# Optimization experiments

Hardware: AMD Instinct MI355X
Metric: run time of the kernel (lower is better)

Reference implementation:

```python
import jax, jax.numpy as jnp
import numpy as np
from jax import lax

HW = 96  # heatmap / image size, hardcoded in the module


def _conv(x, w, b, stride):
    # torch Conv2d: weight [O,I,kH,kW], padding=1
    y = lax.conv_general_dilated(x, w, (stride, stride), [(1, 1), (1, 1)],
                                 dimension_numbers=('NCHW', 'OIHW', 'NCHW'))
    return y + b[None, :, None, None]


def _deconv(x, w, b):
    # torch ConvTranspose2d(k=4, stride=2, padding=1): weight [I,O,kH,kW]
    # equivalent to conv with lhs_dilation=2, padding=k-1-p=2, flipped kernel, I/O swapped
    wf = jnp.flip(w, (-2, -1)).transpose(1, 0, 2, 3)  # [O,I,4,4]
    y = lax.conv_general_dilated(x, wf, (1, 1), [(2, 2), (2, 2)],
                                 lhs_dilation=(2, 2),
                                 dimension_numbers=('NCHW', 'OIHW', 'NCHW'))
    return y + b[None, :, None, None]


def _heatmap(landmarks_flat):
    # landmarks_flat: [B,T,136] -> vectorized scatter of 68 points per frame
    B, T, _ = landmarks_flat.shape
    BT = B * T
    lm = landmarks_flat.reshape(BT, 68, 2) * (HW - 1)
    idx = lm.astype(jnp.int32)          # torch .long() truncation (coords >= 0)
    x, y = idx[..., 0], idx[..., 1]
    valid = (y >= 0) & (y < HW) & (x >= 0) & (x < HW)
    y_s = jnp.where(valid, y, -1)       # out-of-range -> dropped by scatter
    x_s = jnp.where(valid, x, -1)
    bidx = jnp.broadcast_to(jnp.arange(BT)[:, None], (BT, 68))
    h = jnp.zeros((BT, HW, HW), dtype=landmarks_flat.dtype)
    h = h.at[bidx, y_s, x_s].set(1.0, mode='drop')
    return h[:, None, :, :]             # [BT,1,96,96]


def _forward(identity_image, landmark_sequence, w1, b1, w2, b2, w3, b3, w4, b4):
    B, T, _ = landmark_sequence.shape
    ident = jnp.broadcast_to(identity_image[:, None], (B, T, 3, HW, HW)).reshape(B * T, 3, HW, HW)
    hm = _heatmap(landmark_sequence)
    x = jnp.concatenate([ident, hm], axis=1)          # [BT,4,96,96]
    x = jax.nn.relu(_conv(x, w1, b1, 2))              # [BT,64,48,48]
    x = jax.nn.relu(_conv(x, w2, b2, 2))              # [BT,128,24,24]
    x = jax.nn.relu(_deconv(x, w3, b3))               # [BT,64,48,48]
    x = jnp.tanh(_deconv(x, w4, b4))                  # [BT,3,96,96]
    return x.reshape(B, T, 3, HW, HW)


def setup_inputs() -> dict:
    key = jax.random.key(0)
    ks = jax.random.split(key, 10)
    B, T = 8, 32
    identity_image = jax.random.normal(ks[0], (B, 3, HW, HW), dtype=jnp.float32)
    landmark_sequence = jax.random.uniform(ks[1], (B, T, 136), dtype=jnp.float32)
    s = 0.05
    return {
        'identity_image': identity_image,
        'landmark_sequence': landmark_sequence,
        'w1': jax.random.normal(ks[2], (64, 4, 4, 4), jnp.float32) * s,
        'b1': jnp.zeros((64,), jnp.float32),
        'w2': jax.random.normal(ks[3], (128, 64, 4, 4), jnp.float32) * s,
        'b2': jnp.zeros((128,), jnp.float32),
        'w3': jax.random.normal(ks[4], (128, 64, 4, 4), jnp.float32) * s,  # torch ConvTranspose layout [I,O,kH,kW]
        'b3': jnp.zeros((64,), jnp.float32),
        'w4': jax.random.normal(ks[5], (64, 3, 4, 4), jnp.float32) * s,
        'b4': jnp.zeros((3,), jnp.float32),
    }


def reference(identity_image, landmark_sequence, w1, b1, w2, b2, w3, b3, w4, b4):
    return _forward(identity_image, landmark_sequence, w1, b1, w2, b2, w3, b3, w4, b4)
```

## Files before the change

kernel.cpp:

```cpp
#include <hip/hip_runtime.h>

#define IDENTP_OFF 0u
#define HMP_OFF    470400u
#define ACT1CL_OFF 5488000u
#define ACT3P_OFF  470400u
#define ACT2P_OFF  90684800u
#define W2B_OFF    134987136u
#define W3B_OFF    135249280u
#define W1B_OFF    135642496u
#define W4C_OFF    135650688u

using short8  = __attribute__((ext_vector_type(8))) short;
using floatx4 = __attribute__((ext_vector_type(4))) float;
union UV { uint4 u; short8 s; };

static __device__ __forceinline__ float bf2f(unsigned short u) {
  union { unsigned int i; float f; } v; v.i = ((unsigned int)u) << 16; return v.f;
}
static __device__ __forceinline__ unsigned short f2bf(float f) {
  union { float f; unsigned int i; } v; v.f = f;
  unsigned int x = v.i;
  return (unsigned short)((x + 0x7FFFu + ((x >> 16) & 1u)) >> 16);
}
static __device__ __forceinline__ uint4 pack8(const unsigned short* v) {
  uint4 p;
  p.x = (unsigned)v[0] | ((unsigned)v[1] << 16);
  p.y = (unsigned)v[2] | ((unsigned)v[3] << 16);
  p.z = (unsigned)v[4] | ((unsigned)v[5] << 16);
  p.w = (unsigned)v[6] | ((unsigned)v[7] << 16);
  return p;
}
static __device__ __forceinline__ float ftanh(float x) {
  x = fminf(fmaxf(x, -10.f), 10.f);
  float e = __expf(2.f * x);
  return (e - 1.f) * __builtin_amdgcn_rcpf(e + 1.f);
}

__global__ __launch_bounds__(256) void prep_kernel(
    const float* __restrict__ lm, const float* __restrict__ ident,
    const float* __restrict__ w1, const float* __restrict__ w2,
    const float* __restrict__ w3, const float* __restrict__ w4,
    unsigned short* __restrict__ identp, unsigned short* __restrict__ hmp,
    unsigned short* __restrict__ w1b, unsigned short* __restrict__ w2t,
    unsigned short* __restrict__ w3t, unsigned short* __restrict__ w4c,
    unsigned short* __restrict__ act1cl, unsigned short* __restrict__ act2p) {
  int bid = blockIdx.x, tid = threadIdx.x;
  if (bid < 256) {
    unsigned int* h32 = (unsigned int*)(hmp + bid * 9800);
    for (int i = tid; i < 4900; i += 256) h32[i] = 0u;
    __syncthreads();
    if (tid < 68) {
      float x = lm[bid * 136 + tid * 2 + 0] * 95.0f;
      float y = lm[bid * 136 + tid * 2 + 1] * 95.0f;
      int ix = (int)x, iy = (int)y;
      if (ix >= 0 && ix < 96 && iy >= 0 && iy < 96)
        hmp[bid * 9800 + (iy + 1) * 100 + (ix + 1)] = 0x3F80;
    }
  } else if (bid < 320) {
    int idx = (bid - 256) * 2048 + tid * 8;
    int kk = idx >> 12, rem = idx & 4095;
    int n = rem >> 5, e = rem & 31;
    unsigned short v[8];
#pragma unroll
    for (int j = 0; j < 8; j++) {
      int t = kk * 32 + e + j;
      int tap = t >> 6, ic = t & 63;
      v[j] = f2bf(w2[n * 1024 + ic * 16 + tap]);
    }
    *(uint4*)(w2t + idx) = pack8(v);
  } else if (bid < 416) {
    int idx = (bid - 320) * 2048 + tid * 8;
    int r = idx / 98304;
    int rem2 = idx - r * 98304;
    int kk = rem2 >> 12, rem3 = rem2 & 4095;
    int n = rem3 >> 5, e = rem3 & 31;
    int s = n >> 6, oc = n & 63;
    unsigned short v[8];
#pragma unroll
    for (int j = 0; j < 8; j++) {
      int k = kk * 32 + e + j;
      int tap = k >> 7, ic = k & 127;
      int dh = tap / 3, dw = tap - dh * 3;
      int a = 1 - dh, bb = s + 1 - dw;
      unsigned short val = 0;
      if (bb >= 0 && bb <= 1) {
        int kh = 2 * a + 1 - r, kw = 2 * bb + 1 - s;
        val = f2bf(w3[ic * 1024 + oc * 16 + kh * 4 + kw]);
      }
      v[j] = val;
    }
    *(uint4*)(w3t + idx) = pack8(v);
  } else if (bid < 440) {
    int bci = bid - 416;
    const float* src = ident + bci * 9216;
    unsigned short* dst = identp + bci * 9800;
    for (int i = tid; i < 9800; i += 256) {
      int row = i / 100, col = i - row * 100;
      bool in = (row >= 1) && (row <= 96) && (col >= 1) && (col <= 96);
      dst[i] = in ? f2bf(src[(row - 1) * 96 + (col - 1)]) : (unsigned short)0;
    }
  } else if (bid < 696) {
    unsigned short* base = act1cl + (size_t)(bid - 440) * 166400u;
    for (int c = tid; c < 1568; c += 256) {
      int cell = c >> 3, v = c & 7;
      int row, col;
      if (cell < 50) { row = 0; col = cell; }
      else if (cell < 100) { row = 49; col = cell - 50; }
      else if (cell < 148) { row = cell - 99; col = 0; }
      else { row = cell - 147; col = 49; }
      *(uint4*)(base + (row * 52 + col) * 64 + v * 8) = (uint4){0, 0, 0, 0};
    }
  } else if (bid < 952) {
    uint4* b4p = (uint4*)(act2p + (size_t)(bid - 696) * 86528u);
    uint4 z = {0, 0, 0, 0};
    for (int c = tid; c < 1600; c += 256) {
      int cell = c >> 4, v = c & 15;
      int row, col;
      if (cell < 26) { row = 0; col = cell; }
      else if (cell < 52) { row = 25; col = cell - 26; }
      else if (cell < 76) { row = cell - 51; col = 0; }
      else { row = cell - 75; col = 25; }
      b4p[(row * 26 + col) * 16 + v] = z;
    }
  } else if (bid == 952) {
    int e = tid * 16;
    unsigned short v[16];
#pragma unroll
    for (int q = 0; q < 4; q++) {
      float4 f = *(const float4*)(w1 + e + q * 4);
      v[q * 4 + 0] = f2bf(f.x); v[q * 4 + 1] = f2bf(f.y);
      v[q * 4 + 2] = f2bf(f.z); v[q * 4 + 3] = f2bf(f.w);
    }
    *(uint4*)(w1b + e) = pack8(v);
    *(uint4*)(w1b + e + 8) = pack8(v + 8);
  } else {
    for (int idx = tid; idx < 9216; idx += 256) {
      int n = idx / 576, k = idx - n * 576;
      int t = k >> 6, ic = k & 63;
      int dh = t / 3, dw = t - dh * 3;
      unsigned short val = 0;
      if (n < 12) {
        int cls = n / 3, oc = n - cls * 3;
        int r = cls >> 1, s = cls & 1;
        int a = r - dh + 1, b = s - dw + 1;
        if (a >= 0 && a < 2 && b >= 0 && b < 2) {
          int kh = 2 * a + 1 - r, kw = 2 * b + 1 - s;
          val = f2bf(w4[ic * 48 + oc * 16 + kh * 4 + kw]);
        }
      }
      w4c[idx] = val;
    }
  }
}

__global__ __launch_bounds__(256) void conv1_kernel(
    const unsigned short* __restrict__ identp, const unsigned short* __restrict__ hmp,
    const unsigned short* __restrict__ w1b, const float* __restrict__ b1,
    unsigned short* __restrict__ act1cl) {
  __shared__ unsigned short stage[4608];
  int tid = threadIdx.x;
  int bx = blockIdx.x, bt = blockIdx.y;
  int b = bt >> 5;
  int wave = tid >> 6, lane = tid & 63, quad = lane >> 4, l16 = lane & 15;
  int px0 = bx * 64 + wave * 16;
  int pxa = px0 + l16;
  int oh = pxa / 48, ow = pxa % 48;

  floatx4 acc[4];
#pragma unroll
  for (int nt = 0; nt < 4; nt++) acc[nt] = (floatx4){0.f, 0.f, 0.f, 0.f};

#pragma unroll
  for (int kk = 0; kk < 2; kk++) {
    int k0 = kk * 32 + quad * 8;
    int ic = k0 >> 4, khp = (k0 >> 3) & 1;
    const unsigned short* src = (ic < 3) ? identp + (b * 3 + ic) * 9800
                                         : hmp + bt * 9800;
    const unsigned short* p = src + (2 * oh + khp * 2) * 100 + 2 * ow;
    UV a;
    a.u.x = *(const unsigned int*)(p);
    a.u.y = *(const unsigned int*)(p + 2);
    a.u.z = *(const unsigned int*)(p + 100);
    a.u.w = *(const unsigned int*)(p + 102);
#pragma unroll
    for (int nt = 0; nt < 4; nt++) {
      UV bv;
      bv.u = *(const uint4*)(w1b + (nt * 16 + l16) * 64 + kk * 32 + quad * 8);
      acc[nt] = __builtin_amdgcn_mfma_f32_16x16x32_bf16(a.s, bv.s, acc[nt], 0, 0, 0);
    }
  }

  float bias[4];
#pragma unroll
  for (int nt = 0; nt < 4; nt++) bias[nt] = b1[nt * 16 + l16];
  unsigned short* sw = stage + wave * 1152;
#pragma unroll
  for (int nt = 0; nt < 4; nt++)
#pragma unroll
    for (int reg = 0; reg < 4; reg++) {
      float v = fmaxf(acc[nt][reg] + bias[nt], 0.f);
      sw[(quad * 4 + reg) * 72 + nt * 16 + l16] = f2bf(v);
    }
  __syncthreads();
  int oh0 = px0 / 48, ow0 = px0 % 48;
  unsigned short* gout = act1cl + (size_t)bt * 166400u + ((oh0 + 1) * 52 + ow0 + 1) * 64;
#pragma unroll
  for (int it = 0; it < 8; it++) {
    int pl = it * 2 + (lane >> 5);
    unsigned int v = *(const unsigned int*)(sw + pl * 72 + (lane & 31) * 2);
    *(unsigned int*)(gout + pl * 64 + (lane & 31) * 2) = v;
  }
}

__global__ __launch_bounds__(256, 2) void conv2_kernel(
    const unsigned short* __restrict__ act1cl, const unsigned short* __restrict__ w2t,
    const float* __restrict__ b2, unsigned short* __restrict__ act2p) {
  __shared__ unsigned short Blds[2][128 * 40];
  int tid = threadIdx.x;
  int bx = blockIdx.x, bt = blockIdx.y;
  int wave = tid >> 6, lane = tid & 63, quad = lane >> 4, l16 = lane & 15;
  const unsigned short* frame = act1cl + (size_t)bt * 166400u;
  const unsigned short* abase[3];
#pragma unroll
  for (int mf = 0; mf < 3; mf++) {
    int px = bx * 192 + wave * 48 + mf * 16 + l16;
    int oh = px / 24, ow = px % 24;
    abase[mf] = frame + ((2 * oh) * 52 + 2 * ow) * 64 + quad * 8;
  }
  const unsigned short* bptr = w2t + tid * 16;
  unsigned short* sdst = &Blds[0][0] + (tid >> 1) * 40 + (tid & 1) * 16;

  floatx4 acc[3][8];
#pragma unroll
  for (int mf = 0; mf < 3; mf++)
#pragma unroll
    for (int nt = 0; nt < 8; nt++) acc[mf][nt] = (floatx4){0.f, 0.f, 0.f, 0.f};

  {
    uint4 s0 = *(const uint4*)(bptr);
    uint4 s1 = *(const uint4*)(bptr + 8);
    *(uint4*)(sdst) = s0;
    *(uint4*)(sdst + 8) = s1;
  }
  UV a_cur[3], a_nxt[3];
#pragma unroll
  for (int mf = 0; mf < 3; mf++) a_cur[mf].u = *(const uint4*)(abase[mf]);
  __syncthreads();

#pragma unroll 2
  for (int kk = 0; kk < 32; kk++) {
    int cur = kk & 1;
    UV bf[8];
#pragma unroll
    for (int nt = 0; nt < 8; nt++)
      bf[nt].u = *(const uint4*)(&Blds[cur][(nt * 16 + l16) * 40 + quad * 8]);
    uint4 ns0, ns1;
    if (kk < 31) {
      const unsigned short* p = bptr + (kk + 1) * 4096;
      ns0 = *(const uint4*)(p);
      ns1 = *(const uint4*)(p + 8);
      int tap = (kk + 1) >> 1, ic0 = ((kk + 1) & 1) * 32;
      int kh = tap >> 2, kw = tap & 3;
      int aoff = (kh * 52 + kw) * 64 + ic0;
#pragma unroll
      for (int mf = 0; mf < 3; mf++) a_nxt[mf].u = *(const uint4*)(abase[mf] + aoff);
    }
#pragma unroll
    for (int mf = 0; mf < 3; mf++)
#pragma unroll
      for (int nt = 0; nt < 8; nt++)
        acc[mf][nt] = __builtin_amdgcn_mfma_f32_16x16x32_bf16(a_cur[mf].s, bf[nt].s, acc[mf][nt], 0, 0, 0);
    if (kk < 31) {
      unsigned short* d = sdst + (1 - cur) * 5120;
      *(uint4*)(d) = ns0;
      *(uint4*)(d + 8) = ns1;
    }
    __syncthreads();
#pragma unroll
    for (int mf = 0; mf < 3; mf++) a_cur[mf] = a_nxt[mf];
  }

  float bias[8];
#pragma unroll
  for (int nt = 0; nt < 8; nt++) bias[nt] = b2[nt * 16 + l16];
  unsigned short* sw = &Blds[0][0] + wave * 2176;
  unsigned short* obase = act2p + (size_t)bt * 86528u;
#pragma unroll
  for (int mf = 0; mf < 3; mf++) {
#pragma unroll
    for (int nt = 0; nt < 8; nt++)
#pragma unroll
      for (int reg = 0; reg < 4; reg++) {
        float v = fmaxf(acc[mf][nt][reg] + bias[nt], 0.f);
        sw[(quad * 4 + reg) * 136 + nt * 16 + l16] = f2bf(v);
      }
    __syncthreads();
#pragma unroll
    for (int it = 0; it < 16; it++) {
      unsigned int v = *(const unsigned int*)(sw + it * 136 + lane * 2);
      int px = bx * 192 + wave * 48 + mf * 16 + it;
      int oh = px / 24, ow = px % 24;
      *(unsigned int*)(obase + ((oh + 1) * 26 + ow + 1) * 128 + lane * 2) = v;
    }
    __syncthreads();
  }
}

__global__ __launch_bounds__(256, 2) void deconv3_kernel(
    const unsigned short* __restrict__ act2p, const unsigned short* __restrict__ w3t,
    const float* __restrict__ b3, unsigned short* __restrict__ act3p) {
  __shared__ unsigned short Blds[2][128 * 40];
  int tid = threadIdx.x;
  int bx = blockIdx.x, r = blockIdx.y, bt = blockIdx.z;
  int wave = tid >> 6, lane = tid & 63, quad = lane >> 4, l16 = lane & 15;
  const unsigned short* a2 = act2p + (size_t)bt * 86528u;
  unsigned short* a3 = act3p + (size_t)bt * 160000u;

  if (bx == 0 && r == 0) {
    uint4* hz = (uint4*)a3;
    uint4 z = {0, 0, 0, 0};
    for (int c = tid; c < 1568; c += 256) {
      int cell = c >> 3, v = c & 7;
      int row, col;
      if (cell < 50) { row = 0; col = cell; }
      else if (cell < 100) { row = 49; col = cell - 50; }
      else if (cell < 148) { row = cell - 99; col = 0; }
      else { row = cell - 147; col = 49; }
      hz[(row * 50 + col) * 8 + v] = z;
    }
  }

  const unsigned short* abase[3];
#pragma unroll
  for (int mf = 0; mf < 3; mf++) {
    int px = bx * 192 + wave * 48 + mf * 16 + l16;
    int i = px / 24, j = px % 24;
    abase[mf] = a2 + ((i + r) * 26 + j) * 128 + quad * 8;
  }
  const unsigned short* bptr = w3t + r * 98304 + tid * 16;
  unsigned short* sdst = &Blds[0][0] + (tid >> 1) * 40 + (tid & 1) * 16;

  floatx4 acc[3][8];
#pragma unroll
  for (int mf = 0; mf < 3; mf++)
#pragma unroll
    for (int nt = 0; nt < 8; nt++) acc[mf][nt] = (floatx4){0.f, 0.f, 0.f, 0.f};

  {
    uint4 s0 = *(const uint4*)(bptr);
    uint4 s1 = *(const uint4*)(bptr + 8);
    *(uint4*)(sdst) = s0;
    *(uint4*)(sdst + 8) = s1;
  }
  UV a_cur[3], a_nxt[3];
#pragma unroll
  for (int mf = 0; mf < 3; mf++) a_cur[mf].u = *(const uint4*)(abase[mf]);
  __syncthreads();

#pragma unroll 2
  for (int kk = 0; kk < 24; kk++) {
    int cur = kk & 1;
    UV bf[8];
#pragma unroll
    for (int nt = 0; nt < 8; nt++)
      bf[nt].u = *(const uint4*)(&Blds[cur][(nt * 16 + l16) * 40 + quad * 8]);
    uint4 ns0, ns1;
    if (kk < 23) {
      const unsigned short* p = bptr + (kk + 1) * 4096;
      ns0 = *(const uint4*)(p);
      ns1 = *(const uint4*)(p + 8);
      int tap = (kk + 1) >> 2, ic0 = ((kk + 1) & 3) * 32;
      int dh = tap / 3, dw = tap - dh * 3;
      int aoff = (dh * 26 + dw) * 128 + ic0;
#pragma unroll
      for (int mf = 0; mf < 3; mf++) a_nxt[mf].u = *(const uint4*)(abase[mf] + aoff);
    }
#pragma unroll
    for (int mf = 0; mf < 3; mf++)
#pragma unroll
      for (int nt = 0; nt < 8; nt++)
        acc[mf][nt] = __builtin_amdgcn_mfma_f32_16x16x32_bf16(a_cur[mf].s, bf[nt].s, acc[mf][nt], 0, 0, 0);
    if (kk < 23) {
      unsigned short* d = sdst + (1 - cur) * 5120;
      *(uint4*)(d) = ns0;
      *(uint4*)(d + 8) = ns1;
    }
    __syncthreads();
#pragma unroll
    for (int mf = 0; mf < 3; mf++) a_cur[mf] = a_nxt[mf];
  }

  float bias[8];
#pragma unroll
  for (int nt = 0; nt < 8; nt++) bias[nt] = b3[(nt * 16 + l16) & 63];
  unsigned short* sw = &Blds[0][0] + wave * 2176;
#pragma unroll
  for (int mf = 0; mf < 3; mf++) {
#pragma unroll
    for (int nt = 0; nt < 8; nt++)
#pragma unroll
      for (int reg = 0; reg < 4; reg++) {
        float v = fmaxf(acc[mf][nt][reg] + bias[nt], 0.f);
        sw[(quad * 4 + reg) * 136 + nt * 16 + l16] = f2bf(v);
      }
    __syncthreads();
#pragma unroll
    for (int it = 0; it < 16; it++) {
      unsigned int v = *(const unsigned int*)(sw + it * 136 + lane * 2);
      int px = bx * 192 + wave * 48 + mf * 16 + it;
      int i = px / 24, j = px % 24;
      *(unsigned int*)(a3 + ((2 * i + r + 1) * 50 + 2 * j + 1) * 64 + lane * 2) = v;
    }
    __syncthreads();
  }
}

__global__ __launch_bounds__(256) void deconv4_kernel(
    const unsigned short* __restrict__ act3p, const unsigned short* __restrict__ w4c,
    const float* __restrict__ b4, float* __restrict__ out) {
  __shared__ uint4 lds4[2400 + 1168];
  int tid = threadIdx.x;
  int wave = tid >> 6, lane = tid & 63, quad = lane >> 4, l16 = lane & 15;
  int bx = blockIdx.x, bt = blockIdx.y;
  int i0 = bx * 4;

  const uint4* src = (const uint4*)(act3p + (size_t)bt * 160000u + i0 * 3200);
#pragma unroll
  for (int v = 0; v < 10; v++) {
    int g = v * 256 + tid;
    if (g < 2400) {
      uint4 d = src[g];
      int row = g / 400;
      int rem = g - row * 400;
      int rec = rem >> 3, lc = rem & 7;
      lds4[row * 400 + rec * 8 + ((lc + rec) & 7)] = d;
    }
  }
  const uint4* wsrc = (const uint4*)w4c;
#pragma unroll
  for (int v = 0; v < 5; v++) {
    int g = v * 256 + tid;
    if (g < 1152) {
      uint4 d = wsrc[g];
      int n = g / 72, off = g - n * 72;
      lds4[2400 + n * 73 + off] = d;
    }
  }
  __syncthreads();

  const char* alds = (const char*)lds4;
  const char* blds = (const char*)(lds4 + 2400);

  UV bfr[18];
#pragma unroll
  for (int kk = 0; kk < 18; kk++)
    bfr[kk].u = *(const uint4*)(blds + l16 * 1168 + kk * 64 + quad * 16);

  int i = i0 + wave;
  int n = l16;
  int cls = n / 3, oc = n - cls * 3;
  int r = cls >> 1, s = cls & 1;
  float bias = (n < 12) ? b4[oc] : 0.f;
  int oh = 2 * i + r;

#pragma unroll
  for (int t3 = 0; t3 < 3; t3++) {
    int j0 = t3 * 16;
    floatx4 acc = (floatx4){0.f, 0.f, 0.f, 0.f};
#pragma unroll
    for (int kk = 0; kk < 18; kk++) {
      int par = kk & 1, tap = kk >> 1;
      int dh = tap / 3, dw = tap - dh * 3;
      int rec = j0 + dw + l16;
      int pc = (par * 4 + quad + rec) & 7;
      UV a;
      a.u = *(const uint4*)(alds + (wave + dh) * 6400 + rec * 128 + pc * 16);
      acc = __builtin_amdgcn_mfma_f32_16x16x32_bf16(a.s, bfr[kk].s, acc, 0, 0, 0);
    }
    if (n < 12) {
      float* obase = out + (size_t)bt * 27648u + oc * 9216 + oh * 96 + s;
#pragma unroll
      for (int reg = 0; reg < 4; reg++) {
        int jj = j0 + quad * 4 + reg;
        obase[2 * jj] = ftanh(acc[reg] + bias);
      }
    }
  }
}

extern "C" void kernel_launch(void* const* d_in, const int* in_sizes, int n_in,
                              void* d_out, int out_size, void* d_ws, size_t ws_size,
                              hipStream_t stream) {
  const float* ident = (const float*)d_in[0];
  const float* lm = (const float*)d_in[1];
  const float* w1 = (const float*)d_in[2];
  const float* b1 = (const float*)d_in[3];
  const float* w2 = (const float*)d_in[4];
  const float* b2 = (const float*)d_in[5];
  const float* w3 = (const float*)d_in[6];
  const float* b3 = (const float*)d_in[7];
  const float* w4 = (const float*)d_in[8];
  const float* b4 = (const float*)d_in[9];
  float* out = (float*)d_out;
  char* ws = (char*)d_ws;
  unsigned short* identp = (unsigned short*)(ws + IDENTP_OFF);
  unsigned short* hmp = (unsigned short*)(ws + HMP_OFF);
  unsigned short* act1cl = (unsigned short*)(ws + ACT1CL_OFF);
  unsigned short* act2p = (unsigned short*)(ws + ACT2P_OFF);
  unsigned short* act3p = (unsigned short*)(ws + ACT3P_OFF);
  unsigned short* w2t = (unsigned short*)(ws + W2B_OFF);
  unsigned short* w3t = (unsigned short*)(ws + W3B_OFF);
  unsigned short* w1b = (unsigned short*)(ws + W1B_OFF);
  unsigned short* w4c = (unsigned short*)(ws + W4C_OFF);

  prep_kernel<<<dim3(954), 256, 0, stream>>>(lm, ident, w1, w2, w3, w4, identp, hmp,
                                             w1b, w2t, w3t, w4c, act1cl, act2p);
  conv1_kernel<<<dim3(36, 256), 256, 0, stream>>>(identp, hmp, w1b, b1, act1cl);
  conv2_kernel<<<dim3(3, 256), 256, 0, stream>>>(act1cl, w2t, b2, act2p);
  deconv3_kernel<<<dim3(3, 2, 256), 256, 0, stream>>>(act2p, w3t, b3, act3p);
  deconv4_kernel<<<dim3(12, 256), 256, 0, stream>>>(act3p, w4c, b4, out);
}
```

Before: 319.3 us.

## Split deconv3 into four parity-class GEMMs with 2x2 taps, skipping zero-weight taps

The deconv3 kernel previously handled each output-row parity with a 3x3 tap window over both column parities, so its K dimension was padded with zeros. It now launches one block per (row parity, column parity) class using only the 4 real taps, which cuts K from 768 to 512 and N from 128 to 64 per block. The weight prep is rewritten to produce these per-class 2x2 weight matrices. Each class's weights are staged into LDS in two halves instead of a per-step double buffer, the launch grid becomes 12x256, and the 2-blocks-per-CU launch bound is dropped. In exchange there are more blocks, each doing less MFMA work per A-fragment load.

```diff
diff --git a/kernel.cpp b/kernel.cpp
--- a/kernel.cpp
+++ b/kernel.cpp
@@ -42,7 +42,7 @@
     const float* __restrict__ w3, const float* __restrict__ w4,
     unsigned short* __restrict__ identp, unsigned short* __restrict__ hmp,
     unsigned short* __restrict__ w1b, unsigned short* __restrict__ w2t,
-    unsigned short* __restrict__ w3t, unsigned short* __restrict__ w4c,
+    unsigned short* __restrict__ w3c, unsigned short* __restrict__ w4c,
     unsigned short* __restrict__ act1cl, unsigned short* __restrict__ act2p) {
   int bid = blockIdx.x, tid = threadIdx.x;
   if (bid < 256) {
@@ -68,28 +68,26 @@
       v[j] = f2bf(w2[n * 1024 + ic * 16 + tap]);
     }
     *(uint4*)(w2t + idx) = pack8(v);
+  } else if (bid < 384) {
+    int idx = (bid - 320) * 2048 + tid * 8;
+    int c = idx >> 15;
+    int rem = idx & 32767;
+    int kk = rem >> 11;
+    int rem2 = rem & 2047;
+    int n = rem2 >> 5;
+    int ep = rem2 & 31;
+    int r = c >> 1, s = c & 1;
+    unsigned short v[8];
+#pragma unroll
+    for (int j = 0; j < 8; j++) {
+      int k = kk * 32 + ep + j;
+      int tap = k >> 7, ic = k & 127;
+      int dh = tap >> 1, dw = tap & 1;
+      int kh = 3 - r - 2 * dh, kw = 3 - s - 2 * dw;
+      v[j] = f2bf(w3[ic * 1024 + n * 16 + kh * 4 + kw]);
+    }
+    *(uint4*)(w3c + idx) = pack8(v);
   } else if (bid < 416) {
-    int idx = (bid - 320) * 2048 + tid * 8;
-    int r = idx / 98304;
-    int rem2 = idx - r * 98304;
-    int kk = rem2 >> 12, rem3 = rem2 & 4095;
-    int n = rem3 >> 5, e = rem3 & 31;
-    int s = n >> 6, oc = n & 63;
-    unsigned short v[8];
-#pragma unroll
-    for (int j = 0; j < 8; j++) {
-      int k = kk * 32 + e + j;
-      int tap = k >> 7, ic = k & 127;
-      int dh = tap / 3, dw = tap - dh * 3;
-      int a = 1 - dh, bb = s + 1 - dw;
-      unsigned short val = 0;
-      if (bb >= 0 && bb <= 1) {
-        int kh = 2 * a + 1 - r, kw = 2 * bb + 1 - s;
-        val = f2bf(w3[ic * 1024 + oc * 16 + kh * 4 + kw]);
-      }
-      v[j] = val;
-    }
-    *(uint4*)(w3t + idx) = pack8(v);
   } else if (bid < 440) {
     int bci = bid - 416;
     const float* src = ident + bci * 9216;
@@ -306,21 +304,24 @@
   }
 }
 
-__global__ __launch_bounds__(256, 2) void deconv3_kernel(
-    const unsigned short* __restrict__ act2p, const unsigned short* __restrict__ w3t,
+__global__ __launch_bounds__(256) void deconv3_kernel(
+    const unsigned short* __restrict__ act2p, const unsigned short* __restrict__ w3c,
     const float* __restrict__ b3, unsigned short* __restrict__ act3p) {
-  __shared__ unsigned short Blds[2][128 * 40];
+  __shared__ uint4 lds[2560];
   int tid = threadIdx.x;
-  int bx = blockIdx.x, r = blockIdx.y, bt = blockIdx.z;
   int wave = tid >> 6, lane = tid & 63, quad = lane >> 4, l16 = lane & 15;
+
+  int bxc = blockIdx.x, bt = blockIdx.y;
+  int c = bxc & 3, bx = bxc >> 2;
+  int r = c >> 1, s = c & 1;
   const unsigned short* a2 = act2p + (size_t)bt * 86528u;
   unsigned short* a3 = act3p + (size_t)bt * 160000u;
 
-  if (bx == 0 && r == 0) {
+  if (bxc == 0) {
     uint4* hz = (uint4*)a3;
     uint4 z = {0, 0, 0, 0};
-    for (int c = tid; c < 1568; c += 256) {
-      int cell = c >> 3, v = c & 7;
+    for (int cc = tid; cc < 1568; cc += 256) {
+      int cell = cc >> 3, v = cc & 7;
       int row, col;
       if (cell < 50) { row = 0; col = cell; }
       else if (cell < 100) { row = 49; col = cell - 50; }
@@ -334,82 +335,98 @@
 #pragma unroll
   for (int mf = 0; mf < 3; mf++) {
     int px = bx * 192 + wave * 48 + mf * 16 + l16;
-    int i = px / 24, j = px % 24;
-    abase[mf] = a2 + ((i + r) * 26 + j) * 128 + quad * 8;
-  }
-  const unsigned short* bptr = w3t + r * 98304 + tid * 16;
-  unsigned short* sdst = &Blds[0][0] + (tid >> 1) * 40 + (tid & 1) * 16;
-
-  floatx4 acc[3][8];
+    int i = px / 24, j = px - (px / 24) * 24;
+    abase[mf] = a2 + ((i + r) * 26 + (j + s)) * 128 + quad * 8;
+  }
+
+  floatx4 acc[3][4];
 #pragma unroll
   for (int mf = 0; mf < 3; mf++)
 #pragma unroll
-    for (int nt = 0; nt < 8; nt++) acc[mf][nt] = (floatx4){0.f, 0.f, 0.f, 0.f};
+    for (int nt = 0; nt < 4; nt++) acc[mf][nt] = (floatx4){0.f, 0.f, 0.f, 0.f};
+
+  const unsigned short* Bl = (const unsigned short*)lds;
 
   {
-    uint4 s0 = *(const uint4*)(bptr);
-    uint4 s1 = *(const uint4*)(bptr + 8);
-    *(uint4*)(sdst) = s0;
-    *(uint4*)(sdst + 8) = s1;
+    const uint4* gw = (const uint4*)(w3c + c * 32768);
+#pragma unroll
+    for (int v = 0; v < 8; v++) {
+      int g = v * 256 + tid;
+      uint4 d = gw[g];
+      int kkl = g >> 8, r8 = g & 255;
+      int row = r8 >> 2, q = r8 & 3;
+      lds[kkl * 320 + row * 5 + q] = d;
+    }
   }
   UV a_cur[3], a_nxt[3];
 #pragma unroll
   for (int mf = 0; mf < 3; mf++) a_cur[mf].u = *(const uint4*)(abase[mf]);
   __syncthreads();
 
-#pragma unroll 2
-  for (int kk = 0; kk < 24; kk++) {
-    int cur = kk & 1;
-    UV bf[8];
-#pragma unroll
-    for (int nt = 0; nt < 8; nt++)
-      bf[nt].u = *(const uint4*)(&Blds[cur][(nt * 16 + l16) * 40 + quad * 8]);
-    uint4 ns0, ns1;
-    if (kk < 23) {
-      const unsigned short* p = bptr + (kk + 1) * 4096;
-      ns0 = *(const uint4*)(p);
-      ns1 = *(const uint4*)(p + 8);
-      int tap = (kk + 1) >> 2, ic0 = ((kk + 1) & 3) * 32;
-      int dh = tap / 3, dw = tap - dh * 3;
-      int aoff = (dh * 26 + dw) * 128 + ic0;
-#pragma unroll
-      for (int mf = 0; mf < 3; mf++) a_nxt[mf].u = *(const uint4*)(abase[mf] + aoff);
-    }
-#pragma unroll
-    for (int mf = 0; mf < 3; mf++)
-#pragma unroll
-      for (int nt = 0; nt < 8; nt++)
-        acc[mf][nt] = __builtin_amdgcn_mfma_f32_16x16x32_bf16(a_cur[mf].s, bf[nt].s, acc[mf][nt], 0, 0, 0);
-    if (kk < 23) {
-      unsigned short* d = sdst + (1 - cur) * 5120;
-      *(uint4*)(d) = ns0;
-      *(uint4*)(d + 8) = ns1;
-    }
-    __syncthreads();
-#pragma unroll
-    for (int mf = 0; mf < 3; mf++) a_cur[mf] = a_nxt[mf];
-  }
-
-  float bias[8];
-#pragma unroll
-  for (int nt = 0; nt < 8; nt++) bias[nt] = b3[(nt * 16 + l16) & 63];
-  unsigned short* sw = &Blds[0][0] + wave * 2176;
+#pragma unroll
+  for (int half = 0; half < 2; half++) {
+    if (half == 1) {
+      __syncthreads();
+      const uint4* gw = (const uint4*)(w3c + c * 32768 + 16384);
+#pragma unroll
+      for (int v = 0; v < 8; v++) {
+        int g = v * 256 + tid;
+        uint4 d = gw[g];
+        int kkl = g >> 8, r8 = g & 255;
+        int row = r8 >> 2, q = r8 & 3;
+        lds[kkl * 320 + row * 5 + q] = d;
+      }
+      __syncthreads();
+    }
+#pragma unroll
+    for (int kl = 0; kl < 8; kl++) {
+      int kk = half * 8 + kl;
+      UV bf[4];
+#pragma unroll
+      for (int nt = 0; nt < 4; nt++)
+        bf[nt].u = *(const uint4*)(Bl + kl * 2560 + (nt * 16 + l16) * 40 + quad * 8);
+      if (kk < 15) {
+        int kn = kk + 1;
+        int tap = kn >> 2;
+        int aoff = (((tap >> 1) * 26 + (tap & 1)) * 128) + (kn & 3) * 32;
+#pragma unroll
+        for (int mf = 0; mf < 3; mf++) a_nxt[mf].u = *(const uint4*)(abase[mf] + aoff);
+      }
+#pragma unroll
+      for (int mf = 0; mf < 3; mf++)
+#pragma unroll
+        for (int nt = 0; nt < 4; nt++)
+          acc[mf][nt] = __builtin_amdgcn_mfma_f32_16x16x32_bf16(a_cur[mf].s, bf[nt].s, acc[mf][nt], 0, 0, 0);
+#pragma unroll
+      for (int mf = 0; mf < 3; mf++) a_cur[mf] = a_nxt[mf];
+    }
+  }
+
+  float bias[4];
+#pragma unroll
+  for (int nt = 0; nt < 4; nt++) bias[nt] = b3[nt * 16 + l16];
+
+  __syncthreads();
+
+  unsigned short* sw = (unsigned short*)lds + wave * 1152;
 #pragma unroll
   for (int mf = 0; mf < 3; mf++) {
 #pragma unroll
-    for (int nt = 0; nt < 8; nt++)
+    for (int nt = 0; nt < 4; nt++)
 #pragma unroll
       for (int reg = 0; reg < 4; reg++) {
         float v = fmaxf(acc[mf][nt][reg] + bias[nt], 0.f);
-        sw[(quad * 4 + reg) * 136 + nt * 16 + l16] = f2bf(v);
+        sw[(quad * 4 + reg) * 72 + nt * 16 + l16] = f2bf(v);
       }
     __syncthreads();
-#pragma unroll
-    for (int it = 0; it < 16; it++) {
-      unsigned int v = *(const unsigned int*)(sw + it * 136 + lane * 2);
-      int px = bx * 192 + wave * 48 + mf * 16 + it;
-      int i = px / 24, j = px % 24;
-      *(unsigned int*)(a3 + ((2 * i + r + 1) * 50 + 2 * j + 1) * 64 + lane * 2) = v;
+    int pxt = bx * 192 + wave * 48 + mf * 16;
+#pragma unroll
+    for (int it = 0; it < 8; it++) {
+      int p = it * 2 + (lane >> 5);
+      int px = pxt + p;
+      int i = px / 24, j = px - (px / 24) * 24;
+      unsigned int v = *(const unsigned int*)(sw + p * 72 + (lane & 31) * 2);
+      *(unsigned int*)(a3 + ((2 * i + r + 1) * 50 + (2 * j + s + 1)) * 64 + (lane & 31) * 2) = v;
     }
     __syncthreads();
   }
@@ -509,14 +526,14 @@
   unsigned short* act2p = (unsigned short*)(ws + ACT2P_OFF);
   unsigned short* act3p = (unsigned short*)(ws + ACT3P_OFF);
   unsigned short* w2t = (unsigned short*)(ws + W2B_OFF);
-  unsigned short* w3t = (unsigned short*)(ws + W3B_OFF);
+  unsigned short* w3c = (unsigned short*)(ws + W3B_OFF);
   unsigned short* w1b = (unsigned short*)(ws + W1B_OFF);
   unsigned short* w4c = (unsigned short*)(ws + W4C_OFF);
 
   prep_kernel<<<dim3(954), 256, 0, stream>>>(lm, ident, w1, w2, w3, w4, identp, hmp,
-                                             w1b, w2t, w3t, w4c, act1cl, act2p);
+                                             w1b, w2t, w3c, w4c, act1cl, act2p);
   conv1_kernel<<<dim3(36, 256), 256, 0, stream>>>(identp, hmp, w1b, b1, act1cl);
   conv2_kernel<<<dim3(3, 256), 256, 0, stream>>>(act1cl, w2t, b2, act2p);
-  deconv3_kernel<<<dim3(3, 2, 256), 256, 0, stream>>>(act2p, w3t, b3, act3p);
+  deconv3_kernel<<<dim3(12, 256), 256, 0, stream>>>(act2p, w3c, b3, act3p);
   deconv4_kernel<<<dim3(12, 256), 256, 0, stream>>>(act3p, w4c, b4, out);
 }
```

Result: no change. 324.7 us (+1.7%).
